# Kernel optimization log

Hardware: AMD Instinct MI355X
Metric: run time of the kernel (lower is better)

## Reference

```python
import jax, jax.numpy as jnp
import numpy as np

S, B, D, NH, DH, L, V, DI = 1024, 4, 768, 12, 64, 4, 32000, 3072


def layer_norm(x, g, b, eps=1e-5):
    mu = jnp.mean(x, axis=-1, keepdims=True)
    var = jnp.mean((x - mu) ** 2, axis=-1, keepdims=True)
    return (x - mu) * jax.lax.rsqrt(var + eps) * g + b


def sinusoid_pos_emb():
    # PositionalEmbedding: ger(pos_seq, inv_freq) then [sin, cos]
    pos_seq = jnp.arange(S - 1, -1, -1, dtype=jnp.float32)
    inv_freq = 1.0 / (10000.0 ** (jnp.arange(0.0, D, 2.0) / D))
    si = pos_seq[:, None] * inv_freq[None, :]
    return jnp.concatenate([jnp.sin(si), jnp.cos(si)], axis=-1)  # (S, D)


def setup_inputs() -> dict:
    key = jax.random.key(0)
    ks = jax.random.split(key, 16)
    w = 0.02
    inp = jax.random.randint(ks[0], (S, B), 0, V)
    word_emb = jax.random.normal(ks[1], (V, D)) * w
    Wq = jax.random.normal(ks[2], (L, D, D)) * w
    Wkv = jax.random.normal(ks[3], (L, 2 * D, D)) * w
    Wo = jax.random.normal(ks[4], (L, D, D)) * w
    ln1_g = jnp.ones((L, D)); ln1_b = jnp.zeros((L, D))
    ffW1 = jax.random.normal(ks[5], (L, DI, D)) * w
    ffb1 = jnp.zeros((L, DI))
    ffW2 = jax.random.normal(ks[6], (L, D, DI)) * w
    ffb2 = jnp.zeros((L, D))
    ln2_g = jnp.ones((L, D)); ln2_b = jnp.zeros((L, D))
    # pre-populated InfiniAttn memory state; norm kept strictly positive
    memory = jax.random.normal(ks[7], (L, B, NH, DH, DH)) * jnp.sqrt(jnp.float32(S))
    mem_norm = jax.random.uniform(ks[8], (L, B, NH, DH)) * S + 0.5 * S
    return dict(inp=inp, word_emb=word_emb, Wq=Wq, Wkv=Wkv, Wo=Wo,
                ln1_g=ln1_g, ln1_b=ln1_b, ffW1=ffW1, ffb1=ffb1,
                ffW2=ffW2, ffb2=ffb2, ln2_g=ln2_g, ln2_b=ln2_b,
                memory=memory, mem_norm=mem_norm)


def reference(inp, word_emb, Wq, Wkv, Wo, ln1_g, ln1_b, ffW1, ffb1, ffW2, ffb2,
              ln2_g, ln2_b, memory, mem_norm):
    emb_scale = D ** 0.5
    h = word_emb[inp] * emb_scale + sinusoid_pos_emb()[:, None, :]  # (S,B,D)
    causal = jnp.triu(jnp.ones((S, S), dtype=bool), k=1)  # mask j > i
    scale = 1.0 / DH ** 0.5
    gate = jax.nn.sigmoid(jnp.float32(0.01))  # sigmoid(beta), beta_eps=0.01 (buffer)
    neg_inf = jnp.finfo(h.dtype).min
    new_mems, new_norms = [], []
    for l in range(L):
        q = (h @ Wq[l].T).reshape(S, B, NH, DH)
        kv = h @ Wkv[l].T
        k, v = jnp.split(kv, 2, axis=-1)
        k = k.reshape(S, B, NH, DH)
        v = v.reshape(S, B, NH, DH)
        score = jnp.einsum('ibnd,jbnd->ijbn', q, k) * scale
        score = jnp.where(causal[:, :, None, None], neg_inf, score)
        prob = jax.nn.softmax(score, axis=1)
        attn_vec = jnp.einsum('ijbn,jbnd->ibnd', prob, v).reshape(S, B, NH * DH)
        # NOTE: original calls _update_memory(head_q, head_v, head_k), i.e. K=v, V=k
        Qb = jnp.swapaxes(q, 0, 1)  # (B,S,n,d)
        Kb = jnp.swapaxes(v, 0, 1)
        Vb = jnp.swapaxes(k, 0, 1)
        cQ = jax.nn.elu(Qb) + 1.0
        cK = jax.nn.elu(Kb) + 1.0
        # memory retrieval (detached in the original)
        num = jnp.einsum('bsnk,bnkv->bsnv', cQ, memory[l])
        den = jnp.einsum('bsnk,bnk->bsn', cQ, mem_norm[l])[..., None]
        content_A = jax.lax.stop_gradient(num / den)  # (B,S,n,d)
        # memory update with delta trick (no_grad in the original)
        numK = jnp.einsum('bsnk,bnkv->bsnv', cK, memory[l])
        denK = jnp.einsum('bsnk,bnk->bsn', cK, mem_norm[l])[..., None]
        delta = numK / denK
        new_mems.append(jax.lax.stop_gradient(
            memory[l] + jnp.einsum('bsnk,bsnv->bnkv', cK, Vb - delta)))
        new_norms.append(jax.lax.stop_gradient(mem_norm[l] + cK.sum(axis=1)))
        # gated injection of memory content into local attention output
        attn_vec = gate * jnp.swapaxes(content_A, 0, 1).reshape(S, B, NH * DH) \
                   + (1.0 - gate) * attn_vec
        out = layer_norm(h + attn_vec @ Wo[l].T, ln1_g[l], ln1_b[l])
        core = jax.nn.relu(out @ ffW1[l].T + ffb1[l]) @ ffW2[l].T + ffb2[l]
        h = layer_norm(out + core, ln2_g[l], ln2_b[l])
    return h, jnp.stack(new_mems), jnp.stack(new_norms)
```

## Files before the change

### kernel.cpp

```cpp
#include <hip/hip_runtime.h>
#include <hip/hip_bf16.h>
#include <math.h>

#define S 1024
#define B 4
#define Dm 768
#define NH 12
#define DH 64
#define NL 4
#define DI 3072
#define QS 2304
#define MU_CHUNK 8

typedef __hip_bfloat16 bf16;
typedef short bf16x8 __attribute__((ext_vector_type(8)));
typedef float f32x4 __attribute__((ext_vector_type(4)));

__device__ __forceinline__ float b2f(bf16 x) { return __bfloat162float(x); }
__device__ __forceinline__ bf16 f2b(float x) { return __float2bfloat16(x); }

__device__ __forceinline__ float ldv(const float* p, size_t i) { return p[i]; }
__device__ __forceinline__ float ldv(const bf16* p, size_t i) { return b2f(p[i]); }

__device__ __forceinline__ float wave_sum(float x) {
  #pragma unroll
  for (int off = 32; off > 0; off >>= 1) x += __shfl_xor(x, off, 64);
  return x;
}

typedef const __attribute__((address_space(1))) unsigned int guint;
typedef __attribute__((address_space(3))) unsigned int luint;
__device__ __forceinline__ void async_cp16(const void* g, void* l) {
  __builtin_amdgcn_global_load_lds((guint*)g, (luint*)l, 16, 0, 0);
}

__global__ void embed_kernel(const int* __restrict__ inp, const float* __restrict__ wemb,
                             float* __restrict__ h, bf16* __restrict__ hb) {
  int idx = blockIdx.x * blockDim.x + threadIdx.x;
  if (idx >= S * B * Dm) return;
  int d = idx % Dm;
  int sb = idx / Dm;
  int b = sb % B;
  int s = sb / B;
  int tok = inp[s * B + b];
  float e = wemb[(size_t)tok * Dm + d] * 27.712812921102035f;
  float ps = (float)(S - 1 - s);
  float pe;
  if (d < Dm / 2) {
    float invf = expf(-(2.0f * (float)d / (float)Dm) * 9.210340371976184f);
    pe = sinf(ps * invf);
  } else {
    int j = d - Dm / 2;
    float invf = expf(-(2.0f * (float)j / (float)Dm) * 9.210340371976184f);
    pe = cosf(ps * invf);
  }
  float val = e + pe;
  h[idx] = val;
  hb[idx] = f2b(val);
}

#define SEG_QKV 1769472
#define SEG_WO  2359296
#define SEG_W1  4718592
#define SEG_END 7077888
__global__ void convw_kernel(const float* __restrict__ Wq, const float* __restrict__ Wkv,
                             const float* __restrict__ Wo, const float* __restrict__ W1,
                             const float* __restrict__ W2, bf16* __restrict__ dst) {
  int idx = (blockIdx.x * blockDim.x + threadIdx.x) * 4;
  if (idx >= SEG_END) return;
  const float* src;
  if (idx < SEG_QKV) {
    src = (idx < 589824) ? Wq + idx : Wkv + (idx - 589824);
  } else if (idx < SEG_WO) {
    src = Wo + (idx - SEG_QKV);
  } else if (idx < SEG_W1) {
    src = W1 + (idx - SEG_WO);
  } else {
    src = W2 + (idx - SEG_W1);
  }
  float4 f = *(const float4*)src;
  bf16 b0 = f2b(f.x), b1 = f2b(f.y), b2 = f2b(f.z), b3 = f2b(f.w);
  unsigned short o[4];
  o[0] = *(unsigned short*)&b0; o[1] = *(unsigned short*)&b1;
  o[2] = *(unsigned short*)&b2; o[3] = *(unsigned short*)&b3;
  *(uint2*)((unsigned short*)dst + idx) = *(uint2*)o;
}

template <int MREP, int RELU, int SPLITK, typename OT>
__global__ __launch_bounds__(256) void gemm_async(const bf16* __restrict__ A,
                                                  const bf16* __restrict__ W,
                                                  const float* __restrict__ bias,
                                                  OT* __restrict__ C,
                                                  int ldc, int K) {
  constexpr int BM = MREP * 32;
  __shared__ __align__(16) unsigned short Asm[2][BM * 32];
  __shared__ __align__(16) unsigned short Bsm[2][128 * 32];
  const int t = threadIdx.x;
  const int w = t >> 6, lane = t & 63;
  const int col = lane & 15, quad = lane >> 4;
  const int wm = w >> 1, wn = w & 1;
  const int m0 = blockIdx.y * BM, n0 = blockIdx.x * 128;
  const int Kc = K / SPLITK;
  const int kbeg = (SPLITK > 1) ? blockIdx.z * Kc : 0;

  const bf16* aSrc = A + (size_t)(m0 + w * 16 + col) * K + kbeg + quad * 8;
  const bf16* bSrc = W + (size_t)(n0 + w * 16 + col) * K + kbeg + quad * 8;

  const f32x4 zf = {0.0f, 0.0f, 0.0f, 0.0f};
  f32x4 acc[MREP][4];
  #pragma unroll
  for (int mt = 0; mt < MREP; mt++)
    #pragma unroll
    for (int nt = 0; nt < 4; nt++) acc[mt][nt] = zf;

  #pragma unroll
  for (int i = 0; i < MREP / 2; i++)
    async_cp16(aSrc + (size_t)i * 64 * K, &Asm[0][i * 2048 + w * 512]);
  #pragma unroll
  for (int i = 0; i < 2; i++)
    async_cp16(bSrc + (size_t)i * 64 * K, &Bsm[0][i * 2048 + w * 512]);
  __syncthreads();

  int cur = 0;
  for (int kk = 32; kk < Kc; kk += 32) {
    #pragma unroll
    for (int i = 0; i < MREP / 2; i++)
      async_cp16(aSrc + kk + (size_t)i * 64 * K, &Asm[cur ^ 1][i * 2048 + w * 512]);
    #pragma unroll
    for (int i = 0; i < 2; i++)
      async_cp16(bSrc + kk + (size_t)i * 64 * K, &Bsm[cur ^ 1][i * 2048 + w * 512]);
    bf16x8 af[MREP], bfr[4];
    #pragma unroll
    for (int mt = 0; mt < MREP; mt++)
      af[mt] = *(const bf16x8*)&Asm[cur][(wm * MREP + mt) * 512 + lane * 8];
    #pragma unroll
    for (int nt = 0; nt < 4; nt++)
      bfr[nt] = *(const bf16x8*)&Bsm[cur][(wn * 4 + nt) * 512 + lane * 8];
    #pragma unroll
    for (int mt = 0; mt < MREP; mt++)
      #pragma unroll
      for (int nt = 0; nt < 4; nt++)
        acc[mt][nt] = __builtin_amdgcn_mfma_f32_16x16x32_bf16(af[mt], bfr[nt],
                                                              acc[mt][nt], 0, 0, 0);
    __syncthreads();
    cur ^= 1;
  }
  {
    bf16x8 af[MREP], bfr[4];
    #pragma unroll
    for (int mt = 0; mt < MREP; mt++)
      af[mt] = *(const bf16x8*)&Asm[cur][(wm * MREP + mt) * 512 + lane * 8];
    #pragma unroll
    for (int nt = 0; nt < 4; nt++)
      bfr[nt] = *(const bf16x8*)&Bsm[cur][(wn * 4 + nt) * 512 + lane * 8];
    #pragma unroll
    for (int mt = 0; mt < MREP; mt++)
      #pragma unroll
      for (int nt = 0; nt < 4; nt++)
        acc[mt][nt] = __builtin_amdgcn_mfma_f32_16x16x32_bf16(af[mt], bfr[nt],
                                                              acc[mt][nt], 0, 0, 0);
  }

  OT* Cb = C;
  if (SPLITK > 1)
    Cb = C + (size_t)blockIdx.z * gridDim.y * BM * ldc;
  #pragma unroll
  for (int nt = 0; nt < 4; nt++) {
    const int colg = n0 + wn * 64 + nt * 16 + col;
    const float bv = bias ? bias[colg] : 0.0f;
    #pragma unroll
    for (int mt = 0; mt < MREP; mt++) {
      #pragma unroll
      for (int r = 0; r < 4; r++) {
        const int row = m0 + wm * (MREP * 16) + mt * 16 + quad * 4 + r;
        float val = acc[mt][nt][r] + bv;
        if (RELU) val = fmaxf(val, 0.0f);
        if constexpr (__is_same(OT, float)) {
          Cb[(size_t)row * ldc + colg] = val;
        } else {
          Cb[(size_t)row * ldc + colg] = f2b(val);
        }
      }
    }
  }
}

template <int NSLICE, int RELU>
__global__ void gemmred_kernel(const float* __restrict__ part, const float* __restrict__ bias,
                               bf16* __restrict__ out, int N, size_t MN) {
  size_t i4 = ((size_t)blockIdx.x * blockDim.x + threadIdx.x) * 4;
  if (i4 >= MN) return;
  float4 a = *(const float4*)(part + i4);
  #pragma unroll
  for (int z = 1; z < NSLICE; z++) {
    float4 p = *(const float4*)(part + (size_t)z * MN + i4);
    a.x += p.x; a.y += p.y; a.z += p.z; a.w += p.w;
  }
  if (bias) {
    int colb = (int)(i4 % N);
    a.x += bias[colb]; a.y += bias[colb + 1]; a.z += bias[colb + 2]; a.w += bias[colb + 3];
  }
  if (RELU) {
    a.x = fmaxf(a.x, 0.0f); a.y = fmaxf(a.y, 0.0f);
    a.z = fmaxf(a.z, 0.0f); a.w = fmaxf(a.w, 0.0f);
  }
  bf16 b0 = f2b(a.x), b1 = f2b(a.y), b2 = f2b(a.z), b3 = f2b(a.w);
  unsigned short o[4];
  o[0] = *(unsigned short*)&b0; o[1] = *(unsigned short*)&b1;
  o[2] = *(unsigned short*)&b2; o[3] = *(unsigned short*)&b3;
  *(uint2*)((unsigned short*)out + i4) = *(uint2*)o;
}

__global__ __launch_bounds__(256) void attn_flash(const bf16* __restrict__ q,
                                                  const bf16* __restrict__ k,
                                                  const bf16* __restrict__ v,
                                                  bf16* __restrict__ att) {
  const int it = blockIdx.x;
  const int bn = blockIdx.y;
  const int b = bn / NH, n = bn % NH;
  const int t = threadIdx.x;
  const int w = t >> 6, lane = t & 63;
  const int col = lane & 15, quad = lane >> 4;
  const int i0 = it * 64;

  __shared__ __align__(16) unsigned short Kt[64 * 72];
  __shared__ __align__(16) unsigned short Vt[64 * 72];
  __shared__ __align__(16) unsigned short Pw[64 * 72];

  const unsigned short* qp = (const unsigned short*)q;
  const unsigned short* kp = (const unsigned short*)k;
  const unsigned short* vp = (const unsigned short*)v;

  bf16x8 aq[2];
  {
    size_t qb = ((size_t)(i0 + w * 16 + col) * B + b) * QS + n * DH + quad * 8;
    aq[0] = *(const bf16x8*)(qp + qb);
    aq[1] = *(const bf16x8*)(qp + qb + 32);
  }

  const f32x4 zf = {0.0f, 0.0f, 0.0f, 0.0f};
  float mrow[4], lrow[4];
  f32x4 o[4];
  #pragma unroll
  for (int r = 0; r < 4; r++) { mrow[r] = -1e30f; lrow[r] = 0.0f; }
  #pragma unroll
  for (int db = 0; db < 4; db++) o[db] = zf;

  const int jj = t >> 2;
  const int d0 = (t & 3) << 4;

  for (int jt = 0; jt <= it; jt++) {
    const int j0 = jt * 64;
    __syncthreads();
    {
      size_t gb = ((size_t)(j0 + jj) * B + b) * QS + n * DH + d0;
      *(uint4*)&Kt[jj * 72 + d0] = *(const uint4*)(kp + gb);
      *(uint4*)&Kt[jj * 72 + d0 + 8] = *(const uint4*)(kp + gb + 8);
      unsigned short tv[16];
      *(uint4*)tv = *(const uint4*)(vp + gb);
      *(uint4*)(tv + 8) = *(const uint4*)(vp + gb + 8);
      #pragma unroll
      for (int x = 0; x < 16; x++) Vt[(d0 + x) * 72 + jj] = tv[x];
    }
    __syncthreads();

    f32x4 sf[4];
    #pragma unroll
    for (int nb = 0; nb < 4; nb++) sf[nb] = zf;
    #pragma unroll
    for (int ks = 0; ks < 2; ks++) {
      #pragma unroll
      for (int nb = 0; nb < 4; nb++) {
        bf16x8 kb = *(const bf16x8*)&Kt[(nb * 16 + col) * 72 + ks * 32 + quad * 8];
        sf[nb] = __builtin_amdgcn_mfma_f32_16x16x32_bf16(aq[ks], kb, sf[nb], 0, 0, 0);
      }
    }

    const bool diag = (jt == it);
    #pragma unroll
    for (int r = 0; r < 4; r++) {
      const int irow = i0 + w * 16 + quad * 4 + r;
      float sv[4];
      #pragma unroll
      for (int nb = 0; nb < 4; nb++) {
        float s = sf[nb][r] * 0.125f;
        if (diag && (j0 + nb * 16 + col) > irow) s = -1e30f;
        sv[nb] = s;
      }
      float rm = fmaxf(fmaxf(sv[0], sv[1]), fmaxf(sv[2], sv[3]));
      #pragma unroll
      for (int off = 8; off > 0; off >>= 1) rm = fmaxf(rm, __shfl_xor(rm, off, 64));
      const float mn = fmaxf(mrow[r], rm);
      const float alpha = __expf(mrow[r] - mn);
      mrow[r] = mn;
      float ps = 0.0f;
      #pragma unroll
      for (int nb = 0; nb < 4; nb++) {
        float p = __expf(sv[nb] - mn);
        ps += p;
        bf16 hb = f2b(p);
        Pw[(w * 16 + quad * 4 + r) * 72 + nb * 16 + col] = *(unsigned short*)&hb;
      }
      #pragma unroll
      for (int off = 8; off > 0; off >>= 1) ps += __shfl_xor(ps, off, 64);
      lrow[r] = lrow[r] * alpha + ps;
      #pragma unroll
      for (int db = 0; db < 4; db++) o[db][r] *= alpha;
    }

    #pragma unroll
    for (int ks = 0; ks < 2; ks++) {
      bf16x8 pa = *(const bf16x8*)&Pw[(w * 16 + col) * 72 + ks * 32 + quad * 8];
      #pragma unroll
      for (int db = 0; db < 4; db++) {
        bf16x8 vb = *(const bf16x8*)&Vt[(db * 16 + col) * 72 + ks * 32 + quad * 8];
        o[db] = __builtin_amdgcn_mfma_f32_16x16x32_bf16(pa, vb, o[db], 0, 0, 0);
      }
    }
  }

  unsigned short* ap = (unsigned short*)att;
  #pragma unroll
  for (int r = 0; r < 4; r++) {
    const int irow = i0 + w * 16 + quad * 4 + r;
    const float inv = 1.0f / lrow[r];
    size_t ob = ((size_t)irow * B + b) * Dm + n * DH + col;
    #pragma unroll
    for (int db = 0; db < 4; db++) {
      bf16 hb = f2b(o[db][r] * inv);
      ap[ob + db * 16] = *(unsigned short*)&hb;
    }
  }
}

__global__ __launch_bounds__(256) void meminfer_mfma(const bf16* __restrict__ qkv,
                                                     const float* __restrict__ mem,
                                                     const float* __restrict__ mnorm,
                                                     bf16* __restrict__ att,
                                                     bf16* __restrict__ vd) {
  const int s0 = blockIdx.x * 64;
  const int bn = blockIdx.y;
  const int b = bn / NH, n = bn % NH;
  const int t = threadIdx.x;
  const int w = t >> 6, lane = t & 63;
  const int col = lane & 15, quad = lane >> 4;

  __shared__ __align__(16) unsigned short CQ[4096];
  __shared__ __align__(16) unsigned short CK[4096];
  __shared__ __align__(16) unsigned short Bm[5120];

  const unsigned short* qp = (const unsigned short*)qkv;

  {
    int r = t >> 2;
    int k0 = (t & 3) * 16;
    size_t gb = ((size_t)(s0 + r) * B + b) * QS + n * DH + k0;
    int abase = (r >> 4) * 1024 + (k0 >> 5) * 512 + ((k0 & 31) >> 3) * 128 + (r & 15) * 8;
    unsigned short tq[16], tv[16], oq[16], ov[16];
    *(uint4*)tq = *(const uint4*)(qp + gb);
    *(uint4*)(tq + 8) = *(const uint4*)(qp + gb + 8);
    *(uint4*)tv = *(const uint4*)(qp + gb + 1536);
    *(uint4*)(tv + 8) = *(const uint4*)(qp + gb + 1536 + 8);
    #pragma unroll
    for (int i = 0; i < 16; i++) {
      float fq = b2f(*(const bf16*)&tq[i]);
      float fv = b2f(*(const bf16*)&tv[i]);
      float eq = fq > 0.0f ? fq + 1.0f : __expf(fq);
      float ev = fv > 0.0f ? fv + 1.0f : __expf(fv);
      bf16 bq = f2b(eq), bv2 = f2b(ev);
      oq[i] = *(unsigned short*)&bq;
      ov[i] = *(unsigned short*)&bv2;
    }
    *(bf16x8*)&CQ[abase] = *(bf16x8*)oq;
    *(bf16x8*)&CQ[abase + 128] = *(bf16x8*)(oq + 8);
    *(bf16x8*)&CK[abase] = *(bf16x8*)ov;
    *(bf16x8*)&CK[abase + 128] = *(bf16x8*)(ov + 8);
  }
  {
    int v = t & 63, kb = (t >> 6) * 16;
    const float* mp = mem + (size_t)bn * DH * DH;
    #pragma unroll
    for (int i = 0; i < 16; i++) {
      int k = kb + i;
      bf16 mb = f2b(mp[(size_t)k * DH + v]);
      int addr = (v >> 4) * 1024 + (k >> 5) * 512 + ((k & 31) >> 3) * 128 + (v & 15) * 8 + (k & 7);
      Bm[addr] = *(unsigned short*)&mb;
    }
  }
  {
    int a = t * 4;
    int m = (a >> 3) & 15;
    int kk = (a >> 9) * 32 + ((a >> 7) & 3) * 8 + (a & 7);
    unsigned short vals[4] = {0, 0, 0, 0};
    if (m == 0) {
      const float* np = mnorm + (size_t)bn * DH;
      #pragma unroll
      for (int j = 0; j < 4; j++) {
        bf16 nb = f2b(np[kk + j]);
        vals[j] = *(unsigned short*)&nb;
      }
    }
    *(uint2*)&Bm[4096 + a] = *(uint2*)vals;
  }
  __syncthreads();

  const f32x4 zf = {0.0f, 0.0f, 0.0f, 0.0f};
  f32x4 aq[5], ak[5];
  #pragma unroll
  for (int nb = 0; nb < 5; nb++) { aq[nb] = zf; ak[nb] = zf; }
  #pragma unroll
  for (int ks = 0; ks < 2; ks++) {
    bf16x8 fq = *(const bf16x8*)&CQ[w * 1024 + ks * 512 + lane * 8];
    bf16x8 fk = *(const bf16x8*)&CK[w * 1024 + ks * 512 + lane * 8];
    #pragma unroll
    for (int nb = 0; nb < 5; nb++) {
      bf16x8 bm = *(const bf16x8*)&Bm[nb * 1024 + ks * 512 + lane * 8];
      aq[nb] = __builtin_amdgcn_mfma_f32_16x16x32_bf16(fq, bm, aq[nb], 0, 0, 0);
      ak[nb] = __builtin_amdgcn_mfma_f32_16x16x32_bf16(fk, bm, ak[nb], 0, 0, 0);
    }
  }

  const float gate = 1.0f / (1.0f + expf(-0.01f));
  unsigned short* ap = (unsigned short*)att;
  unsigned short* vp2 = (unsigned short*)vd;
  #pragma unroll
  for (int r = 0; r < 4; r++) {
    const int srow = s0 + w * 16 + quad * 4 + r;
    const float denq = __shfl(aq[4][r], lane & 48, 64);
    const float denk = __shfl(ak[4][r], lane & 48, 64);
    const size_t bd = ((size_t)srow * B + b) * Dm + n * DH + col;
    const size_t bq = ((size_t)srow * B + b) * QS + 768 + n * DH + col;
    #pragma unroll
    for (int nb = 0; nb < 4; nb++) {
      float content = aq[nb][r] / denq;
      float delta = ak[nb][r] / denk;
      float attv = b2f(*(const bf16*)&ap[bd + nb * 16]);
      bf16 ao = f2b(gate * content + (1.0f - gate) * attv);
      ap[bd + nb * 16] = *(unsigned short*)&ao;
      float kvv = b2f(*(const bf16*)&qp[bq + nb * 16]);
      bf16 vo = f2b(kvv - delta);
      vp2[bd + nb * 16] = *(unsigned short*)&vo;
    }
  }
}

__global__ void memupd_kernel(const bf16* __restrict__ qkv, const bf16* __restrict__ vd,
                              float* __restrict__ part, float* __restrict__ pnorm) {
  int bn = blockIdx.x % (B * NH);
  int c = blockIdx.x / (B * NH);
  int b = bn / NH, n = bn % NH;
  int t = threadIdx.x;
  int k = t >> 2;
  int v0 = (t & 3) * 16;
  __shared__ float ckl[8][DH];
  __shared__ float vdl[8][DH];
  float acc[16];
  #pragma unroll
  for (int j = 0; j < 16; j++) acc[j] = 0.0f;
  float nsum = 0.0f;
  const int sBeg = c * (S / MU_CHUNK), sEnd = sBeg + S / MU_CHUNK;
  for (int s0 = sBeg; s0 < sEnd; s0 += 8) {
    #pragma unroll
    for (int i2 = 0; i2 < 2; i2++) {
      int idx = t + i2 * 256;
      int sp = idx >> 6, dd = idx & 63;
      int gq = ((s0 + sp) * B + b) * QS + 1536 + n * DH + dd;
      int gd = ((s0 + sp) * B + b) * Dm + n * DH + dd;
      float vv = b2f(qkv[gq]);
      ckl[sp][dd] = vv > 0.0f ? vv + 1.0f : expf(vv);
      vdl[sp][dd] = b2f(vd[gd]);
    }
    __syncthreads();
    #pragma unroll
    for (int sp = 0; sp < 8; sp++) {
      float cc = ckl[sp][k];
      if ((t & 3) == 0) nsum += cc;
      #pragma unroll
      for (int j = 0; j < 16; j++) acc[j] += cc * vdl[sp][v0 + j];
    }
    __syncthreads();
  }
  float* prow = part + (size_t)c * (B * NH * DH * DH) + (size_t)bn * DH * DH;
  #pragma unroll
  for (int j4 = 0; j4 < 4; j4++) {
    float4 o;
    o.x = acc[j4 * 4 + 0]; o.y = acc[j4 * 4 + 1];
    o.z = acc[j4 * 4 + 2]; o.w = acc[j4 * 4 + 3];
    *(float4*)&prow[k * DH + v0 + j4 * 4] = o;
  }
  if ((t & 3) == 0) pnorm[(size_t)c * (B * NH * DH) + bn * DH + k] = nsum;
}

__global__ void memred_kernel(const float* __restrict__ mem, const float* __restrict__ mnorm,
                              const float* __restrict__ part, const float* __restrict__ pnorm,
                              float* __restrict__ out_mem, float* __restrict__ out_norm) {
  const int MEMN = B * NH * DH * DH;
  int i = blockIdx.x * blockDim.x + threadIdx.x;
  if (i < MEMN / 4) {
    int i4 = i * 4;
    float4 a = *(const float4*)(mem + i4);
    #pragma unroll
    for (int c = 0; c < MU_CHUNK; c++) {
      float4 p = *(const float4*)(part + (size_t)c * MEMN + i4);
      a.x += p.x; a.y += p.y; a.z += p.z; a.w += p.w;
    }
    *(float4*)(out_mem + i4) = a;
  } else {
    int j4 = (i - MEMN / 4) * 4;
    if (j4 < B * NH * DH) {
      float4 a = *(const float4*)(mnorm + j4);
      #pragma unroll
      for (int c = 0; c < MU_CHUNK; c++) {
        float4 p = *(const float4*)(pnorm + (size_t)c * (B * NH * DH) + j4);
        a.x += p.x; a.y += p.y; a.z += p.z; a.w += p.w;
      }
      *(float4*)(out_norm + j4) = a;
    }
  }
}

template <typename TX, typename TY>
__global__ void addln_kernel(const TX* __restrict__ x, const TY* __restrict__ y,
                             const float* __restrict__ g, const float* __restrict__ bb,
                             float* __restrict__ outf, bf16* __restrict__ outb) {
  int row = blockIdx.x;
  int t = threadIdx.x;
  float vals[3];
  float sum = 0.0f, sq = 0.0f;
  #pragma unroll
  for (int i = 0; i < 3; i++) {
    size_t idx = (size_t)row * Dm + t + i * 256;
    float vv = ldv(x, idx) + ldv(y, idx);
    vals[i] = vv;
    sum += vv;
    sq += vv * vv;
  }
  sum = wave_sum(sum);
  sq = wave_sum(sq);
  __shared__ float s1[4], s2[4];
  int w = t >> 6, lane = t & 63;
  if (lane == 0) { s1[w] = sum; s2[w] = sq; }
  __syncthreads();
  if (t == 0) {
    s1[0] = s1[0] + s1[1] + s1[2] + s1[3];
    s2[0] = s2[0] + s2[1] + s2[2] + s2[3];
  }
  __syncthreads();
  sum = s1[0]; sq = s2[0];
  float mu = sum / 768.0f;
  float var = sq / 768.0f - mu * mu;
  float rs = rsqrtf(var + 1e-5f);
  #pragma unroll
  for (int i = 0; i < 3; i++) {
    int d = t + i * 256;
    float o = (vals[i] - mu) * rs * g[d] + bb[d];
    size_t idx = (size_t)row * Dm + d;
    if (outf) outf[idx] = o;
    if (outb) outb[idx] = f2b(o);
  }
}

extern "C" void kernel_launch(void* const* d_in, const int* in_sizes, int n_in,
                              void* d_out, int out_size, void* d_ws, size_t ws_size,
                              hipStream_t stream) {
  (void)in_sizes; (void)n_in; (void)out_size;
  const int*   inp   = (const int*)d_in[0];
  const float* wemb  = (const float*)d_in[1];
  const float* Wq    = (const float*)d_in[2];
  const float* Wkv   = (const float*)d_in[3];
  const float* Wo    = (const float*)d_in[4];
  const float* ln1g  = (const float*)d_in[5];
  const float* ln1b  = (const float*)d_in[6];
  const float* fW1   = (const float*)d_in[7];
  const float* fb1   = (const float*)d_in[8];
  const float* fW2   = (const float*)d_in[9];
  const float* fb2   = (const float*)d_in[10];
  const float* ln2g  = (const float*)d_in[11];
  const float* ln2b  = (const float*)d_in[12];
  const float* mem   = (const float*)d_in[13];
  const float* mnorm = (const float*)d_in[14];

  const size_t SBD = (size_t)S * B * Dm;

  bf16* ws   = (bf16*)d_ws;
  bf16* qkv  = ws;
  bf16* vd   = ws + 3 * SBD;
  bf16* att  = ws + 4 * SBD;
  bf16* hbf  = att;
  bf16* ff2o = att;
  bf16* out1 = ws + 5 * SBD;
  bf16* wb   = ws + 6 * SBD;
  bf16* ffm  = ws;
  bf16* tmp  = ws;
  float* part  = (float*)out1;
  float* pnorm = (float*)(wb + SEG_END);
  float* partg = pnorm + (size_t)MU_CHUNK * B * NH * DH;
  const size_t need = ((size_t)(6 * SBD + SEG_END)) * 2 +
                      ((size_t)MU_CHUNK * B * NH * DH + 2 * SBD) * 4;
  const bool use_splitk = (ws_size >= need);

  float* h    = (float*)d_out;
  float* outm = h + SBD;
  float* outn = outm + (size_t)NL * B * NH * DH * DH;

  dim3 b256(256);
  embed_kernel<<<dim3((S * B * Dm + 255) / 256), b256, 0, stream>>>(inp, wemb, h, hbf);

  for (int l = 0; l < NL; l++) {
    convw_kernel<<<dim3(SEG_END / 4 / 256), b256, 0, stream>>>(
        Wq + (size_t)l * Dm * Dm, Wkv + (size_t)l * 2 * Dm * Dm,
        Wo + (size_t)l * Dm * Dm, fW1 + (size_t)l * DI * Dm,
        fW2 + (size_t)l * Dm * DI, wb);
    const bf16* wqkv = wb;
    const bf16* wo_b = wb + SEG_QKV;
    const bf16* w1_b = wb + SEG_WO;
    const bf16* w2_b = wb + SEG_W1;
    const float* mem_l = mem + (size_t)l * B * NH * DH * DH;
    const float* mn_l  = mnorm + (size_t)l * B * NH * DH;
    float* outm_l = outm + (size_t)l * B * NH * DH * DH;
    float* outn_l = outn + (size_t)l * B * NH * DH;

    gemm_async<4, 0, 1, bf16><<<dim3(QS / 128, 32), b256, 0, stream>>>(
        hbf, wqkv, nullptr, qkv, QS, Dm);

    attn_flash<<<dim3(S / 64, B * NH), b256, 0, stream>>>(qkv, qkv + 768, qkv + 1536, att);
    meminfer_mfma<<<dim3(S / 64, B * NH), b256, 0, stream>>>(qkv, mem_l, mn_l, att, vd);
    memupd_kernel<<<dim3(B * NH * MU_CHUNK), b256, 0, stream>>>(qkv, vd, part, pnorm);
    memred_kernel<<<dim3(771), b256, 0, stream>>>(mem_l, mn_l, part, pnorm, outm_l, outn_l);

    if (use_splitk) {
      gemm_async<2, 0, 2, float><<<dim3(Dm / 128, 64, 2), b256, 0, stream>>>(
          att, wo_b, nullptr, partg, Dm, Dm);
      gemmred_kernel<2, 0><<<dim3((unsigned)(SBD / 4 / 256)), b256, 0, stream>>>(
          partg, nullptr, tmp, Dm, SBD);
    } else {
      gemm_async<2, 0, 1, bf16><<<dim3(Dm / 128, 64), b256, 0, stream>>>(
          att, wo_b, nullptr, tmp, Dm, Dm);
    }
    addln_kernel<float, bf16><<<dim3(S * B), b256, 0, stream>>>(
        h, tmp, ln1g + l * Dm, ln1b + l * Dm, nullptr, out1);

    gemm_async<4, 1, 1, bf16><<<dim3(DI / 128, 32), b256, 0, stream>>>(
        out1, w1_b, fb1 + (size_t)l * DI, ffm, DI, Dm);
    if (use_splitk) {
      gemm_async<2, 0, 2, float><<<dim3(Dm / 128, 64, 2), b256, 0, stream>>>(
          ffm, w2_b, nullptr, partg, Dm, DI);
      gemmred_kernel<2, 0><<<dim3((unsigned)(SBD / 4 / 256)), b256, 0, stream>>>(
          partg, fb2 + (size_t)l * Dm, ff2o, Dm, SBD);
    } else {
      gemm_async<2, 0, 1, bf16><<<dim3(Dm / 128, 64), b256, 0, stream>>>(
          ffm, w2_b, fb2 + (size_t)l * Dm, ff2o, Dm, DI);
    }
    addln_kernel<bf16, bf16><<<dim3(S * B), b256, 0, stream>>>(
        out1, ff2o, ln2g + l * Dm, ln2b + l * Dm, h, hbf);
  }
}
```

Baseline: 1.326 ms.

## Split flash attention over KV range and prefetch next K/V tile into registers

Adds a split-KV variant of the causal flash attention kernel. Each query tile's key range is divided into two halves, handled by separate blocks that write partial outputs plus row max and sum. A new combine kernel merges the halves with log-sum-exp weights. This evens out the triangular causal workload and raises the block count. It also register-prefetches the next K/V tile while the current one is computed. The cost is an extra kernel launch, extra global traffic for the partials, and bf16 rounding of the partial outputs before they are combined.

```diff
diff --git a/kernel.cpp b/kernel.cpp
--- a/kernel.cpp
+++ b/kernel.cpp
@@ -11,6 +11,7 @@
 #define DI 3072
 #define QS 2304
 #define MU_CHUNK 8
+#define NROW (S * B * NH)
 
 typedef __hip_bfloat16 bf16;
 typedef short bf16x8 __attribute__((ext_vector_type(8)));
@@ -211,10 +212,14 @@
   *(uint2*)((unsigned short*)out + i4) = *(uint2*)o;
 }
 
+template <int SPLIT>
 __global__ __launch_bounds__(256) void attn_flash(const bf16* __restrict__ q,
                                                   const bf16* __restrict__ k,
                                                   const bf16* __restrict__ v,
-                                                  bf16* __restrict__ att) {
+                                                  bf16* __restrict__ att,
+                                                  bf16* __restrict__ po0,
+                                                  bf16* __restrict__ po1,
+                                                  float* __restrict__ pml) {
   const int it = blockIdx.x;
   const int bn = blockIdx.y;
   const int b = bn / NH, n = bn % NH;
@@ -223,6 +228,13 @@
   const int col = lane & 15, quad = lane >> 4;
   const int i0 = it * 64;
 
+  int jbeg = 0, jend = it + 1;
+  if (SPLIT == 2) {
+    const int half = (it + 2) >> 1;
+    if (blockIdx.z == 0) jend = half; else jbeg = half;
+    if (jbeg >= jend) return;
+  }
+
   __shared__ __align__(16) unsigned short Kt[64 * 72];
   __shared__ __align__(16) unsigned short Vt[64 * 72];
   __shared__ __align__(16) unsigned short Pw[64 * 72];
@@ -249,20 +261,31 @@
   const int jj = t >> 2;
   const int d0 = (t & 3) << 4;
 
-  for (int jt = 0; jt <= it; jt++) {
+  uint4 rk0, rk1, rv0, rv1;
+  {
+    size_t gb = ((size_t)(jbeg * 64 + jj) * B + b) * QS + n * DH + d0;
+    rk0 = *(const uint4*)(kp + gb); rk1 = *(const uint4*)(kp + gb + 8);
+    rv0 = *(const uint4*)(vp + gb); rv1 = *(const uint4*)(vp + gb + 8);
+  }
+
+  for (int jt = jbeg; jt < jend; jt++) {
     const int j0 = jt * 64;
     __syncthreads();
     {
-      size_t gb = ((size_t)(j0 + jj) * B + b) * QS + n * DH + d0;
-      *(uint4*)&Kt[jj * 72 + d0] = *(const uint4*)(kp + gb);
-      *(uint4*)&Kt[jj * 72 + d0 + 8] = *(const uint4*)(kp + gb + 8);
+      *(uint4*)&Kt[jj * 72 + d0] = rk0;
+      *(uint4*)&Kt[jj * 72 + d0 + 8] = rk1;
       unsigned short tv[16];
-      *(uint4*)tv = *(const uint4*)(vp + gb);
-      *(uint4*)(tv + 8) = *(const uint4*)(vp + gb + 8);
+      *(uint4*)tv = rv0;
+      *(uint4*)(tv + 8) = rv1;
       #pragma unroll
       for (int x = 0; x < 16; x++) Vt[(d0 + x) * 72 + jj] = tv[x];
     }
     __syncthreads();
+    if (jt + 1 < jend) {
+      size_t gb = ((size_t)((jt + 1) * 64 + jj) * B + b) * QS + n * DH + d0;
+      rk0 = *(const uint4*)(kp + gb); rk1 = *(const uint4*)(kp + gb + 8);
+      rv0 = *(const uint4*)(vp + gb); rv1 = *(const uint4*)(vp + gb + 8);
+    }
 
     f32x4 sf[4];
     #pragma unroll
@@ -319,18 +342,72 @@
     }
   }
 
-  unsigned short* ap = (unsigned short*)att;
-  #pragma unroll
-  for (int r = 0; r < 4; r++) {
-    const int irow = i0 + w * 16 + quad * 4 + r;
-    const float inv = 1.0f / lrow[r];
-    size_t ob = ((size_t)irow * B + b) * Dm + n * DH + col;
-    #pragma unroll
-    for (int db = 0; db < 4; db++) {
-      bf16 hb = f2b(o[db][r] * inv);
-      ap[ob + db * 16] = *(unsigned short*)&hb;
-    }
-  }
+  if (SPLIT == 1) {
+    unsigned short* ap = (unsigned short*)att;
+    #pragma unroll
+    for (int r = 0; r < 4; r++) {
+      const int irow = i0 + w * 16 + quad * 4 + r;
+      const float inv = 1.0f / lrow[r];
+      size_t ob = ((size_t)irow * B + b) * Dm + n * DH + col;
+      #pragma unroll
+      for (int db = 0; db < 4; db++) {
+        bf16 hb = f2b(o[db][r] * inv);
+        ap[ob + db * 16] = *(unsigned short*)&hb;
+      }
+    }
+  } else {
+    unsigned short* pp = (unsigned short*)(blockIdx.z ? po1 : po0);
+    float* pm = pml + (size_t)blockIdx.z * 2 * NROW;
+    float* pl = pm + NROW;
+    #pragma unroll
+    for (int r = 0; r < 4; r++) {
+      const int irow = i0 + w * 16 + quad * 4 + r;
+      const float inv = 1.0f / lrow[r];
+      size_t ob = ((size_t)irow * B + b) * Dm + n * DH + col;
+      #pragma unroll
+      for (int db = 0; db < 4; db++) {
+        bf16 hb = f2b(o[db][r] * inv);
+        pp[ob + db * 16] = *(unsigned short*)&hb;
+      }
+      if (col == 0) {
+        int rix = (irow * B + b) * NH + n;
+        pm[rix] = mrow[r];
+        pl[rix] = lrow[r];
+      }
+    }
+  }
+}
+
+__global__ void attn_comb(const bf16* __restrict__ po0, const bf16* __restrict__ po1,
+                          const float* __restrict__ pml, bf16* __restrict__ att) {
+  size_t i4 = ((size_t)blockIdx.x * blockDim.x + threadIdx.x) * 4;
+  if (i4 >= (size_t)S * B * Dm) return;
+  int sb = (int)(i4 / Dm);
+  int dd = (int)(i4 % Dm);
+  int srow = sb / B;
+  int it = srow >> 6;
+  uint2 a0 = *(const uint2*)((const unsigned short*)po0 + i4);
+  if (it == 0) {
+    *(uint2*)((unsigned short*)att + i4) = a0;
+    return;
+  }
+  uint2 a1 = *(const uint2*)((const unsigned short*)po1 + i4);
+  int rix = sb * NH + (dd >> 6);
+  float m0 = pml[rix],            l0 = pml[NROW + rix];
+  float m1 = pml[2 * NROW + rix], l1 = pml[3 * NROW + rix];
+  float M = fmaxf(m0, m1);
+  float w0 = l0 * __expf(m0 - M), w1 = l1 * __expf(m1 - M);
+  float inv = 1.0f / (w0 + w1);
+  const unsigned short* p0 = (const unsigned short*)&a0;
+  const unsigned short* p1 = (const unsigned short*)&a1;
+  unsigned short o[4];
+  #pragma unroll
+  for (int j = 0; j < 4; j++) {
+    float val = (w0 * b2f(*(const bf16*)&p0[j]) + w1 * b2f(*(const bf16*)&p1[j])) * inv;
+    bf16 hb = f2b(val);
+    o[j] = *(unsigned short*)&hb;
+  }
+  *(uint2*)((unsigned short*)att + i4) = *(uint2*)o;
 }
 
 __global__ __launch_bounds__(256) void meminfer_mfma(const bf16* __restrict__ qkv,
@@ -598,6 +675,9 @@
   const size_t need = ((size_t)(6 * SBD + SEG_END)) * 2 +
                       ((size_t)MU_CHUNK * B * NH * DH + 2 * SBD) * 4;
   const bool use_splitk = (ws_size >= need);
+  bf16* po0 = vd;
+  bf16* po1 = out1;
+  float* pml = partg;
 
   float* h    = (float*)d_out;
   float* outm = h + SBD;
@@ -623,7 +703,14 @@
     gemm_async<4, 0, 1, bf16><<<dim3(QS / 128, 32), b256, 0, stream>>>(
         hbf, wqkv, nullptr, qkv, QS, Dm);
 
-    attn_flash<<<dim3(S / 64, B * NH), b256, 0, stream>>>(qkv, qkv + 768, qkv + 1536, att);
+    if (use_splitk) {
+      attn_flash<2><<<dim3(S / 64, B * NH, 2), b256, 0, stream>>>(
+          qkv, qkv + 768, qkv + 1536, att, po0, po1, pml);
+      attn_comb<<<dim3((unsigned)(SBD / 4 / 256)), b256, 0, stream>>>(po0, po1, pml, att);
+    } else {
+      attn_flash<1><<<dim3(S / 64, B * NH), b256, 0, stream>>>(
+          qkv, qkv + 768, qkv + 1536, att, nullptr, nullptr, nullptr);
+    }
     meminfer_mfma<<<dim3(S / 64, B * NH), b256, 0, stream>>>(qkv, mem_l, mn_l, att, vd);
     memupd_kernel<<<dim3(B * NH * MU_CHUNK), b256, 0, stream>>>(qkv, vd, part, pnorm);
     memred_kernel<<<dim3(771), b256, 0, stream>>>(mem_l, mn_l, part, pnorm, outm_l, outn_l);
```

Result: no change. 1.338 ms (+0.9%).
